# Kernel optimization log

Measured on AMD Instinct MI355X. Metric: run time of the kernel, lower is better.

## Reference

```python
import jax, jax.numpy as jnp
import numpy as np

D_MODEL = 1024
D_Q = 1024
D_K = 1024
D_V = 1024
B, S = 4, 2048


def setup_inputs() -> dict:
    key = jax.random.key(0)
    kx, kq, kk, kv = jax.random.split(key, 4)
    # torch Linear(in, out) weight is [out, in]; y = x @ W.T. Use kaiming-ish scale.
    sc = 1.0 / np.sqrt(D_MODEL)
    x = jax.random.normal(kx, (B, S, D_MODEL), dtype=jnp.float32)
    Wq = jax.random.normal(kq, (D_Q, D_MODEL), dtype=jnp.float32) * sc
    Wk = jax.random.normal(kk, (D_K, D_MODEL), dtype=jnp.float32) * sc
    Wv = jax.random.normal(kv, (D_V, D_MODEL), dtype=jnp.float32) * sc
    return {"x": x, "Wq": Wq, "Wk": Wk, "Wv": Wv}


def reference(x, Wq, Wk, Wv):
    d_k = Wk.shape[0]
    q = jnp.einsum('bsd,qd->bsq', x, Wq)  # [B,S,d_q]
    k = jnp.einsum('bsd,kd->bsk', x, Wk)  # [B,S,d_k]
    v = jnp.einsum('bsd,vd->bsv', x, Wv)  # [B,S,d_v]
    scores = jnp.einsum('bqd,bkd->bqk', q, k) / jnp.sqrt(jnp.float32(d_k))
    seq = scores.shape[-1]
    causal = jnp.tril(jnp.ones((seq, seq), dtype=bool))  # True = keep
    scores = jnp.where(causal[None, :, :], scores, -jnp.inf)
    probs = jax.nn.softmax(scores, axis=-1)
    return jnp.einsum('bqk,bkv->bqv', probs, v)
```

## Files before the change

kernel.cpp:

```cpp
#include <hip/hip_runtime.h>
#include <hip/hip_bf16.h>
#include <stdint.h>

typedef __attribute__((ext_vector_type(8))) short short8;
typedef __attribute__((ext_vector_type(4))) float floatx4;

typedef const __attribute__((address_space(1))) void* gvp;
typedef __attribute__((address_space(3))) void* lvp;

__device__ __forceinline__ unsigned short f2bf(float f) {
    unsigned u = __float_as_uint(f);
    u += 0x7fffu + ((u >> 16) & 1u);
    return (unsigned short)(u >> 16);
}

#define BAR()   do { asm volatile("" ::: "memory"); __builtin_amdgcn_s_barrier(); asm volatile("" ::: "memory"); } while (0)
#define WAITL() do { asm volatile("s_waitcnt lgkmcnt(0)" ::: "memory"); __builtin_amdgcn_sched_barrier(0); } while (0)
#define WAITV4() asm volatile("s_waitcnt vmcnt(4)" ::: "memory")
#define WAITV0() asm volatile("s_waitcnt vmcnt(0)" ::: "memory")

__global__ __launch_bounds__(256)
void cvt_all(const float* __restrict__ x, const float* __restrict__ wq,
             const float* __restrict__ wk, const float* __restrict__ wv,
             unsigned short* __restrict__ Xb, unsigned short* __restrict__ WqT,
             unsigned short* __restrict__ WkT, unsigned short* __restrict__ Wvb) {
    const int b = blockIdx.x, t = threadIdx.x;
    if (b < 2304) {
        const float* in; unsigned short* out; long base;
        if (b < 2048) { in = x;  out = Xb;  base = (long)b * 1024; }
        else          { in = wv; out = Wvb; base = (long)(b - 2048) * 1024; }
        #pragma unroll
        for (int k = 0; k < 4; ++k) {
            long idx = base + k * 256 + t;
            float4 v = reinterpret_cast<const float4*>(in)[idx];
            uint2 o;
            o.x = (unsigned)f2bf(v.x) | ((unsigned)f2bf(v.y) << 16);
            o.y = (unsigned)f2bf(v.z) | ((unsigned)f2bf(v.w) << 16);
            reinterpret_cast<uint2*>(out)[idx] = o;
        }
    } else {
        const int bb = b - 2304;
        const float* in = (bb < 256) ? wq : wk;
        unsigned short* out = (bb < 256) ? WqT : WkT;
        const int tile = bb & 255;
        const int e0 = (tile >> 4) * 64, d0 = (tile & 15) * 64;
        __shared__ unsigned short ldsT[64][68];
        const int r = t >> 4, cq = t & 15;
        #pragma unroll
        for (int p = 0; p < 4; ++p) {
            const int e = p * 16 + r;
            float4 v = *reinterpret_cast<const float4*>(in + (long)(e0 + e) * 1024 + d0 + cq * 4);
            ldsT[cq*4+0][e] = f2bf(v.x);
            ldsT[cq*4+1][e] = f2bf(v.y);
            ldsT[cq*4+2][e] = f2bf(v.z);
            ldsT[cq*4+3][e] = f2bf(v.w);
        }
        __syncthreads();
        #pragma unroll
        for (int p = 0; p < 4; ++p) {
            const int d = p * 16 + r;
            ushort4 o = *reinterpret_cast<const ushort4*>(&ldsT[d][cq * 4]);
            *reinterpret_cast<ushort4*>(out + (long)(d0 + d) * 1024 + e0 + cq * 4) = o;
        }
    }
}

__device__ __forceinline__ void stage_tile(unsigned short* Abuf, unsigned short* Bbuf,
                                           const unsigned short* A, int lda,
                                           const unsigned short* B, int ldb, int k0,
                                           int wid, int srow, int piece) {
    #pragma unroll
    for (int i = 0; i < 4; ++i) {
        const int c = wid * 4 + i;
        const int row = c * 8 + srow;
        const int cs = (piece * 16) ^ ((row & 7) << 4);
        __builtin_amdgcn_global_load_lds(
            (gvp)(reinterpret_cast<const char*>(A + (long)row * lda + k0) + cs),
            (lvp)(reinterpret_cast<char*>(Abuf) + c * 1024), 16, 0, 0);
        __builtin_amdgcn_global_load_lds(
            (gvp)(reinterpret_cast<const char*>(B + (long)row * ldb + k0) + cs),
            (lvp)(reinterpret_cast<char*>(Bbuf) + c * 1024), 16, 0, 0);
    }
}

__device__ __forceinline__ void compute_tile(floatx4 acc[4][4], const unsigned short* As,
                                             const unsigned short* Bs, int wm, int wn,
                                             int frow, int lane) {
    #pragma unroll
    for (int ks = 0; ks < 2; ++ks) {
        short8 af[4], bf[4];
        const int colb = ks * 64 + (lane >> 4) * 16;
        #pragma unroll
        for (int i = 0; i < 4; ++i) {
            const int ar = wm + i * 16 + frow;
            af[i] = *reinterpret_cast<const short8*>(
                reinterpret_cast<const char*>(As) + ar * 128 + (colb ^ ((ar & 7) << 4)));
            const int br = wn + i * 16 + frow;
            bf[i] = *reinterpret_cast<const short8*>(
                reinterpret_cast<const char*>(Bs) + br * 128 + (colb ^ ((br & 7) << 4)));
        }
        #pragma unroll
        for (int i = 0; i < 4; ++i)
            #pragma unroll
            for (int j = 0; j < 4; ++j)
                acc[i][j] = __builtin_amdgcn_mfma_f32_16x16x32_bf16(af[i], bf[j], acc[i][j], 0, 0, 0);
    }
}

__global__ __launch_bounds__(256, 2)
void g_chunk(const unsigned short* __restrict__ WkT, const unsigned short* __restrict__ WqT,
             float* __restrict__ Gw) {
    const int bx = blockIdx.x, by = blockIdx.y, bz = blockIdx.z;
    const unsigned short* A = WkT + (long)by * 128 * 1024;
    const unsigned short* B = WqT + (long)bx * 128 * 1024;

    __shared__ unsigned short As[2][128 * 64];
    __shared__ unsigned short Bs[2][128 * 64];

    const int tid = threadIdx.x, lane = tid & 63, wid = tid >> 6;
    const int srow = lane >> 3, piece = lane & 7;
    const int wm = (wid >> 1) * 64, wn = (wid & 1) * 64, frow = lane & 15;

    floatx4 acc[4][4] = {};
    const int kbase = bz * 256;

    stage_tile(As[0], Bs[0], A, 1024, B, 1024, kbase, wid, srow, piece);
    WAITV0(); BAR();
    int cur = 0;
    #pragma unroll 1
    for (int t = 0; t < 4; ++t) {
        if (t < 3)
            stage_tile(As[cur ^ 1], Bs[cur ^ 1], A, 1024, B, 1024, kbase + (t + 1) * 64,
                       wid, srow, piece);
        compute_tile(acc, As[cur], Bs[cur], wm, wn, frow, lane);
        WAITV0(); BAR();
        cur ^= 1;
    }

    float* Cb = Gw + (long)bz * (1 << 20) + (long)(by * 128) * 1024 + bx * 128;
    const int cr0 = wm + (lane >> 4) * 4;
    const int cc0 = wn + (lane & 15);
    #pragma unroll
    for (int i = 0; i < 4; ++i)
        #pragma unroll
        for (int j = 0; j < 4; ++j)
            #pragma unroll
            for (int r = 0; r < 4; ++r)
                Cb[(long)(cr0 + i * 16 + r) * 1024 + cc0 + j * 16] = acc[i][j][r];
}

__global__ __launch_bounds__(256)
void reduce_g(const float* __restrict__ Gw, unsigned short* __restrict__ Gp) {
    const long i4 = (long)blockIdx.x * 256 + threadIdx.x;
    const long M4 = (1l << 20) / 4;
    float4 a = reinterpret_cast<const float4*>(Gw)[i4];
    float4 b = reinterpret_cast<const float4*>(Gw)[i4 + M4];
    float4 c = reinterpret_cast<const float4*>(Gw)[i4 + 2 * M4];
    float4 d = reinterpret_cast<const float4*>(Gw)[i4 + 3 * M4];
    float sx = (a.x + b.x + c.x + d.x) * 0.03125f;
    float sy = (a.y + b.y + c.y + d.y) * 0.03125f;
    float sz = (a.z + b.z + c.z + d.z) * 0.03125f;
    float sw = (a.w + b.w + c.w + d.w) * 0.03125f;
    uint2 o;
    o.x = (unsigned)f2bf(sx) | ((unsigned)f2bf(sy) << 16);
    o.y = (unsigned)f2bf(sz) | ((unsigned)f2bf(sw) << 16);
    reinterpret_cast<uint2*>(Gp)[i4] = o;
}

__global__ __launch_bounds__(256, 2)
void pv_pair(const unsigned short* __restrict__ P, const unsigned short* __restrict__ Vt,
             float* __restrict__ out) {
    int flat = (blockIdx.z * 8 + blockIdx.y) * 8 + blockIdx.x;
    { int xcd = flat & 7, lid = flat >> 3; flat = xcd * 32 + lid; }
    const int bx = flat % 8;
    const int pj = (flat / 8) % 8;
    const int bz = flat / 64;

    const unsigned short* Pb = P + (long)bz * 2048 * 4096;
    const unsigned short* Bv = Vt + (long)bz * 1024 * 2048 + (long)(bx * 128) * 2048;
    float* Cb = out + (long)bz * 2048 * 1024;

    __shared__ unsigned short As[2][128 * 64];
    __shared__ unsigned short Bs[2][128 * 64];

    const int tid = threadIdx.x, lane = tid & 63, wid = tid >> 6;
    const int srow = lane >> 3, piece = lane & 7;
    const int wm = (wid >> 1) * 64, wn = (wid & 1) * 64, frow = lane & 15;

    #pragma unroll 1
    for (int j = 0; j < 2; ++j) {
        const int by = j ? 15 - pj : pj;
        const unsigned short* A = Pb + (long)by * 128 * 4096;
        const int nt = (by + 1) * 2;

        floatx4 acc[4][4] = {};
        stage_tile(As[0], Bs[0], A, 4096, Bv, 2048, 0, wid, srow, piece);
        WAITV0(); BAR();
        int cur = 0;
        #pragma unroll 1
        for (int t = 0; t < nt; ++t) {
            if (t + 1 < nt)
                stage_tile(As[cur ^ 1], Bs[cur ^ 1], A, 4096, Bv, 2048, (t + 1) * 64,
                           wid, srow, piece);
            compute_tile(acc, As[cur], Bs[cur], wm, wn, frow, lane);
            WAITV0(); BAR();
            cur ^= 1;
        }

        float* Cj = Cb + (long)(by * 128) * 1024 + bx * 128;
        const int cr0 = wm + (lane >> 4) * 4;
        const int cc0 = wn + (lane & 15);
        #pragma unroll
        for (int i = 0; i < 4; ++i)
            #pragma unroll
            for (int jj = 0; jj < 4; ++jj)
                #pragma unroll
                for (int r = 0; r < 4; ++r)
                    Cj[(long)(cr0 + i * 16 + r) * 1024 + cc0 + jj * 16] = acc[i][jj][r];
    }
}

__device__ __forceinline__ void stage_half(char* slot, const unsigned short* src,
                                           int ld, int k0, int tid) {
    #pragma unroll
    for (int r = 0; r < 2; ++r) {
        const int c = r * 512 + tid;
        const int row = c >> 3;
        const int cs = ((c & 7) * 16) ^ ((row & 7) << 4);
        const char* g = reinterpret_cast<const char*>(src + (long)row * ld + k0) + cs;
        __builtin_amdgcn_global_load_lds((gvp)g,
            (lvp)(slot + r * 8192 + (tid >> 6) * 1024), 16, 0, 0);
    }
}

__device__ __forceinline__ void load_a4(short8 a_[4][2], const char* slot, int mh,
                                        int fr, int csw0, int csw1) {
    #pragma unroll
    for (int i = 0; i < 4; ++i) {
        const int rb = (mh * 64 + i * 16 + fr) * 128;
        a_[i][0] = *reinterpret_cast<const short8*>(slot + rb + csw0);
        a_[i][1] = *reinterpret_cast<const short8*>(slot + rb + csw1);
    }
}

__device__ __forceinline__ void load_b2(short8 b_[2][2], const char* slot, int rbase,
                                        int nh, int fr, int csw0, int csw1) {
    #pragma unroll
    for (int j = 0; j < 2; ++j) {
        const int rb = (rbase + nh * 32 + j * 16 + fr) * 128;
        b_[j][0] = *reinterpret_cast<const short8*>(slot + rb + csw0);
        b_[j][1] = *reinterpret_cast<const short8*>(slot + rb + csw1);
    }
}

__device__ __forceinline__ void mfma16(floatx4 acc[8][4], short8 a_[4][2],
                                       short8 b_[2][2], int mh, int nh) {
    __builtin_amdgcn_s_setprio(1);
    #pragma unroll
    for (int i = 0; i < 4; ++i)
        #pragma unroll
        for (int j = 0; j < 2; ++j) {
            acc[mh*4+i][nh*2+j] = __builtin_amdgcn_mfma_f32_16x16x32_bf16(
                a_[i][0], b_[j][0], acc[mh*4+i][nh*2+j], 0, 0, 0);
            acc[mh*4+i][nh*2+j] = __builtin_amdgcn_mfma_f32_16x16x32_bf16(
                a_[i][1], b_[j][1], acc[mh*4+i][nh*2+j], 0, 0, 0);
        }
    __builtin_amdgcn_s_setprio(0);
}

template<typename CT, int MODE>
__global__ __launch_bounds__(512, 2)
void gemm8p(const unsigned short* __restrict__ A, const unsigned short* B,
            const unsigned short* B1, CT* __restrict__ C, unsigned short* __restrict__ Vt,
            int K, int lda, int ldb, int ldc,
            long sA, long sB, long sC, int nwg)
{
    const int gx = gridDim.x, gy = gridDim.y;
    int flat = (blockIdx.z * gy + blockIdx.y) * gx + blockIdx.x;
    {
        int xcd = flat & 7, lid = flat >> 3;
        int q = nwg >> 3, r = nwg & 7;
        flat = (xcd < r ? xcd * (q + 1) : r * (q + 1) + (xcd - r) * q) + lid;
    }
    int bx, by, bz = 0;
    bool isV = false;
    if (MODE == 1) {
        bx = flat % gx;
        int t2 = flat / gx;
        by = t2 % gy;
        bz = t2 / gy;
        if (bx > by) return;
    } else {
        if (flat >= 128) { isV = true; flat -= 128; B = B1; }
        by = flat >> 2;
        bx = flat & 3;
    }

    A += (long)bz * sA + (long)by * 256 * lda;
    B += (long)bz * sB + (long)bx * 256 * ldb;
    C += (long)bz * sC;

    __shared__ __align__(16) char lds[8 * 16384];
    #define SLOT(db, op, half) (lds + ((((db) << 1 | (op)) << 1 | (half)) * 16384))

    const int tid  = threadIdx.x;
    const int lane = tid & 63;
    const int wid  = tid >> 6;
    const int wm = wid >> 2;
    const int wn = wid & 3;
    const int bh = wn >> 1;
    const int brbase = (wn & 1) * 64;
    const int fr = lane & 15;
    const int csw0 = ((lane >> 4) * 16) ^ ((fr & 7) << 4);
    const int csw1 = (64 + (lane >> 4) * 16) ^ ((fr & 7) << 4);

    const unsigned short* Ah[2] = { A, A + 128ll * lda };
    const unsigned short* Bh[2] = { B, B + 128ll * ldb };

    const int NT = K >> 6;
    const int NI = NT >> 1;

    floatx4 acc[8][4] = {};
    short8 a_[4][2];
    short8 b_[2][2][2];

    stage_half(SLOT(0,1,0), Bh[0], ldb, 0, tid);
    stage_half(SLOT(0,1,1), Bh[1], ldb, 0, tid);
    stage_half(SLOT(0,0,0), Ah[0], lda, 0, tid);
    stage_half(SLOT(0,0,1), Ah[1], lda, 0, tid);
    stage_half(SLOT(1,1,0), Bh[0], ldb, 64, tid);
    stage_half(SLOT(1,1,1), Bh[1], ldb, 64, tid);
    WAITV4();
    BAR();

    for (int I = 0; I < NI; ++I) {
        const int kA1 = min(2*I + 1, NT - 1) * 64;
        const int kT2 = min(2*I + 2, NT - 1) * 64;
        const int kB3 = min(2*I + 3, NT - 1) * 64;

        load_a4(a_, SLOT(0,0,wm), 0, fr, csw0, csw1);
        load_b2(b_[0], SLOT(0,1,bh), brbase, 0, fr, csw0, csw1);
        stage_half(SLOT(1,0,0), Ah[0], lda, kA1, tid);
        BAR(); WAITL();
        mfma16(acc, a_, b_[0], 0, 0);
        BAR();

        load_b2(b_[1], SLOT(0,1,bh), brbase, 1, fr, csw0, csw1);
        stage_half(SLOT(1,0,1), Ah[1], lda, kA1, tid);
        BAR(); WAITL();
        mfma16(acc, a_, b_[1], 0, 1);
        BAR();

        load_a4(a_, SLOT(0,0,wm), 1, fr, csw0, csw1);
        stage_half(SLOT(0,1,0), Bh[0], ldb, kT2, tid);
        BAR(); WAITL();
        mfma16(acc, a_, b_[1], 1, 1);
        BAR();

        stage_half(SLOT(0,1,1), Bh[1], ldb, kT2, tid);
        BAR(); WAITL();
        mfma16(acc, a_, b_[0], 1, 0);
        WAITV4();
        BAR();

        load_a4(a_, SLOT(1,0,wm), 0, fr, csw0, csw1);
        load_b2(b_[0], SLOT(1,1,bh), brbase, 0, fr, csw0, csw1);
        stage_half(SLOT(0,0,0), Ah[0], lda, kT2, tid);
        BAR(); WAITL();
        mfma16(acc, a_, b_[0], 0, 0);
        BAR();

        load_b2(b_[1], SLOT(1,1,bh), brbase, 1, fr, csw0, csw1);
        stage_half(SLOT(0,0,1), Ah[1], lda, kT2, tid);
        BAR(); WAITL();
        mfma16(acc, a_, b_[1], 0, 1);
        BAR();

        load_a4(a_, SLOT(1,0,wm), 1, fr, csw0, csw1);
        stage_half(SLOT(1,1,0), Bh[0], ldb, kB3, tid);
        BAR(); WAITL();
        mfma16(acc, a_, b_[1], 1, 1);
        BAR();

        stage_half(SLOT(1,1,1), Bh[1], ldb, kB3, tid);
        BAR(); WAITL();
        mfma16(acc, a_, b_[0], 1, 0);
        WAITV4();
        BAR();
    }

    if (MODE == 3 && isV) {
        WAITV0();
        BAR();
        char* T = lds;
        #pragma unroll
        for (int i = 0; i < 8; ++i)
            #pragma unroll
            for (int j = 0; j < 4; ++j) {
                const int n = wn * 64 + j * 16 + fr;
                const int m = wm * 128 + ((lane >> 4) << 2) + i * 16;
                uint2 pk;
                pk.x = (unsigned)f2bf(acc[i][j][0]) | ((unsigned)f2bf(acc[i][j][1]) << 16);
                pk.y = (unsigned)f2bf(acc[i][j][2]) | ((unsigned)f2bf(acc[i][j][3]) << 16);
                *reinterpret_cast<uint2*>(T + n * 512 + ((m * 2) ^ ((n & 7) << 4))) = pk;
            }
        __syncthreads();
        const int b  = by >> 3;
        const int s0 = (by & 7) * 256;
        #pragma unroll
        for (int c = 0; c < 16; ++c) {
            const int idx = c * 512 + tid;
            const int n = idx >> 5, k = idx & 31;
            uint4 v = *reinterpret_cast<const uint4*>(T + n * 512 + ((k * 16) ^ ((n & 7) << 4)));
            *reinterpret_cast<uint4*>(Vt + (long)b * (1024 * 2048)
                + (long)(bx * 256 + n) * 2048 + s0 + k * 8) = v;
        }
        return;
    }

    const int cr0 = by * 256 + wm * 128 + (lane >> 4) * 4;
    const int cc0 = bx * 256 + wn * 64 + (lane & 15);
    #pragma unroll
    for (int i = 0; i < 8; ++i)
        #pragma unroll
        for (int j = 0; j < 4; ++j)
            #pragma unroll
            for (int r = 0; r < 4; ++r) {
                long idx = (long)(cr0 + i * 16 + r) * ldc + (cc0 + j * 16);
                float v = acc[i][j][r];
                if constexpr (sizeof(CT) == 4) C[idx] = v;
                else                           C[idx] = (CT)f2bf(v);
            }
    #undef SLOT
}

__global__ __launch_bounds__(256)
void softmax_causal(float* __restrict__ Sc) {
    const int q = blockIdx.x;
    const int b = blockIdx.y;
    float* row = Sc + ((long)b * 2048 + q) * 2048;
    const int t = threadIdx.x;
    const int lane = t & 63, wid = t >> 6;
    const int kend = (q | 127) + 1;

    float vals[8];
    float mx = -INFINITY;
    #pragma unroll
    for (int i = 0; i < 2; ++i) {
        const int c0 = i * 1024 + t * 4;
        if (c0 <= q) {
            float4 v = *reinterpret_cast<const float4*>(row + c0);
            float tmp[4] = {v.x, v.y, v.z, v.w};
            #pragma unroll
            for (int j = 0; j < 4; ++j) {
                float val = (c0 + j <= q) ? tmp[j] : -INFINITY;
                vals[i * 4 + j] = val;
                mx = fmaxf(mx, val);
            }
        } else {
            vals[i*4+0] = vals[i*4+1] = vals[i*4+2] = vals[i*4+3] = -INFINITY;
        }
    }
    #pragma unroll
    for (int o = 32; o > 0; o >>= 1) mx = fmaxf(mx, __shfl_xor(mx, o));
    __shared__ float rmax[4], rsum[4];
    if (lane == 0) rmax[wid] = mx;
    __syncthreads();
    mx = fmaxf(fmaxf(rmax[0], rmax[1]), fmaxf(rmax[2], rmax[3]));

    float s = 0.f;
    #pragma unroll
    for (int k = 0; k < 8; ++k) {
        float e = __expf(vals[k] - mx);
        vals[k] = e;
        s += e;
    }
    #pragma unroll
    for (int o = 32; o > 0; o >>= 1) s += __shfl_xor(s, o);
    if (lane == 0) rsum[wid] = s;
    __syncthreads();
    s = rsum[0] + rsum[1] + rsum[2] + rsum[3];
    const float inv = 1.f / s;

    unsigned short* orow = reinterpret_cast<unsigned short*>(row);
    #pragma unroll
    for (int i = 0; i < 2; ++i) {
        const int c0 = i * 1024 + t * 4;
        if (c0 < kend) {
            uint2 o;
            o.x = (unsigned)f2bf(vals[i*4+0] * inv) | ((unsigned)f2bf(vals[i*4+1] * inv) << 16);
            o.y = (unsigned)f2bf(vals[i*4+2] * inv) | ((unsigned)f2bf(vals[i*4+3] * inv) << 16);
            *reinterpret_cast<uint2*>(orow + c0) = o;
        }
    }
}

extern "C" void kernel_launch(void* const* d_in, const int* in_sizes, int n_in,
                              void* d_out, int out_size, void* d_ws, size_t ws_size,
                              hipStream_t stream) {
    const float* x  = (const float*)d_in[0];
    const float* Wq = (const float*)d_in[1];
    const float* Wk = (const float*)d_in[2];
    const float* Wv = (const float*)d_in[3];
    float* out = (float*)d_out;

    char* w = (char*)d_ws;
    unsigned short* Xb  = (unsigned short*)(w);
    unsigned short* WqT = (unsigned short*)(w + (16ll << 20));
    unsigned short* WkT = (unsigned short*)(w + (18ll << 20));
    unsigned short* Wvb = (unsigned short*)(w + (20ll << 20));
    unsigned short* Yb  = (unsigned short*)(w + (22ll << 20));
    unsigned short* Gp  = (unsigned short*)(w + (38ll << 20));
    float*          Gw  = (float*)(w + (40ll << 20));
    unsigned short* Vt  = (unsigned short*)(w + (70ll << 20));
    float* Sc = (float*)(w + (86ll << 20));

    dim3 blk(256);
    cvt_all<<<2816, blk, 0, stream>>>(x, Wq, Wk, Wv, Xb, WqT, WkT, Wvb);

    g_chunk<<<dim3(8, 8, 4), blk, 0, stream>>>(WkT, WqT, Gw);
    reduce_g<<<1024, blk, 0, stream>>>(Gw, Gp);

    gemm8p<unsigned short, 3><<<dim3(256, 1, 1), dim3(512), 0, stream>>>(
        Xb, Gp, Wvb, Yb, Vt, 1024, 1024, 1024, 1024,
        0, 0, 0, 256);

    gemm8p<float, 1><<<dim3(8, 8, 4), dim3(512), 0, stream>>>(
        Yb, Xb, nullptr, Sc, nullptr, 1024, 1024, 1024, 2048,
        2048ll * 1024, 2048ll * 1024, 2048ll * 2048, 256);

    softmax_causal<<<dim3(2048, 4), blk, 0, stream>>>(Sc);

    pv_pair<<<dim3(8, 8, 4), blk, 0, stream>>>((const unsigned short*)Sc, Vt, out);
}
```

Measured before the change: 145.3 us.

## Deepen PV pipeline to four LDS stages and pair softmax rows per block

```diff
diff --git a/kernel.cpp b/kernel.cpp
--- a/kernel.cpp
+++ b/kernel.cpp
@@ -14,10 +14,12 @@
     return (unsigned short)(u >> 16);
 }
 
-#define BAR()   do { asm volatile("" ::: "memory"); __builtin_amdgcn_s_barrier(); asm volatile("" ::: "memory"); } while (0)
-#define WAITL() do { asm volatile("s_waitcnt lgkmcnt(0)" ::: "memory"); __builtin_amdgcn_sched_barrier(0); } while (0)
+#define BAR()    do { asm volatile("" ::: "memory"); __builtin_amdgcn_s_barrier(); asm volatile("" ::: "memory"); } while (0)
+#define WAITL()  do { asm volatile("s_waitcnt lgkmcnt(0)" ::: "memory"); __builtin_amdgcn_sched_barrier(0); } while (0)
 #define WAITV4() asm volatile("s_waitcnt vmcnt(4)" ::: "memory")
 #define WAITV0() asm volatile("s_waitcnt vmcnt(0)" ::: "memory")
+#define WAITV8() asm volatile("s_waitcnt vmcnt(8)" ::: "memory")
+#define WAITV16() asm volatile("s_waitcnt vmcnt(16)" ::: "memory")
 
 __global__ __launch_bounds__(256)
 void cvt_all(const float* __restrict__ x, const float* __restrict__ wq,
@@ -167,7 +169,7 @@
     reinterpret_cast<uint2*>(Gp)[i4] = o;
 }
 
-__global__ __launch_bounds__(256, 2)
+__global__ __launch_bounds__(256, 1)
 void pv_pair(const unsigned short* __restrict__ P, const unsigned short* __restrict__ Vt,
              float* __restrict__ out) {
     int flat = (blockIdx.z * 8 + blockIdx.y) * 8 + blockIdx.x;
@@ -180,8 +182,8 @@
     const unsigned short* Bv = Vt + (long)bz * 1024 * 2048 + (long)(bx * 128) * 2048;
     float* Cb = out + (long)bz * 2048 * 1024;
 
-    __shared__ unsigned short As[2][128 * 64];
-    __shared__ unsigned short Bs[2][128 * 64];
+    __shared__ unsigned short As[4][128 * 64];
+    __shared__ unsigned short Bs[4][128 * 64];
 
     const int tid = threadIdx.x, lane = tid & 63, wid = tid >> 6;
     const int srow = lane >> 3, piece = lane & 7;
@@ -194,17 +196,25 @@
         const int nt = (by + 1) * 2;
 
         floatx4 acc[4][4] = {};
-        stage_tile(As[0], Bs[0], A, 4096, Bv, 2048, 0, wid, srow, piece);
-        WAITV0(); BAR();
-        int cur = 0;
+        stage_tile(As[0], Bs[0], A, 4096, Bv, 2048, 0,   wid, srow, piece);
+        stage_tile(As[1], Bs[1], A, 4096, Bv, 2048, 64,  wid, srow, piece);
+        stage_tile(As[2], Bs[2], A, 4096, Bv, 2048, 128, wid, srow, piece);
+        WAITV16();
+        BAR();
+
         #pragma unroll 1
         for (int t = 0; t < nt; ++t) {
-            if (t + 1 < nt)
-                stage_tile(As[cur ^ 1], Bs[cur ^ 1], A, 4096, Bv, 2048, (t + 1) * 64,
-                           wid, srow, piece);
-            compute_tile(acc, As[cur], Bs[cur], wm, wn, frow, lane);
-            WAITV0(); BAR();
-            cur ^= 1;
+            if (t + 3 < nt) {
+                stage_tile(As[(t + 3) & 3], Bs[(t + 3) & 3], A, 4096, Bv, 2048,
+                           (t + 3) * 64, wid, srow, piece);
+                compute_tile(acc, As[t & 3], Bs[t & 3], wm, wn, frow, lane);
+                WAITV16();
+            } else {
+                compute_tile(acc, As[t & 3], Bs[t & 3], wm, wn, frow, lane);
+                if (t + 2 < nt)      { WAITV8(); }
+                else                 { WAITV0(); }
+            }
+            BAR();
         }
 
         float* Cj = Cb + (long)(by * 128) * 1024 + bx * 128;
@@ -436,61 +446,65 @@
 
 __global__ __launch_bounds__(256)
 void softmax_causal(float* __restrict__ Sc) {
-    const int q = blockIdx.x;
     const int b = blockIdx.y;
-    float* row = Sc + ((long)b * 2048 + q) * 2048;
     const int t = threadIdx.x;
     const int lane = t & 63, wid = t >> 6;
-    const int kend = (q | 127) + 1;
-
-    float vals[8];
-    float mx = -INFINITY;
-    #pragma unroll
-    for (int i = 0; i < 2; ++i) {
-        const int c0 = i * 1024 + t * 4;
-        if (c0 <= q) {
-            float4 v = *reinterpret_cast<const float4*>(row + c0);
-            float tmp[4] = {v.x, v.y, v.z, v.w};
-            #pragma unroll
-            for (int j = 0; j < 4; ++j) {
-                float val = (c0 + j <= q) ? tmp[j] : -INFINITY;
-                vals[i * 4 + j] = val;
-                mx = fmaxf(mx, val);
+    __shared__ float rmax[2][4], rsum[2][4];
+
+    #pragma unroll 1
+    for (int h = 0; h < 2; ++h) {
+        const int q = h ? 2047 - blockIdx.x : blockIdx.x;
+        float* row = Sc + ((long)b * 2048 + q) * 2048;
+        const int kend = (q | 127) + 1;
+
+        float vals[8];
+        float mx = -INFINITY;
+        #pragma unroll
+        for (int i = 0; i < 2; ++i) {
+            const int c0 = i * 1024 + t * 4;
+            if (c0 <= q) {
+                float4 v = *reinterpret_cast<const float4*>(row + c0);
+                float tmp[4] = {v.x, v.y, v.z, v.w};
+                #pragma unroll
+                for (int j = 0; j < 4; ++j) {
+                    float val = (c0 + j <= q) ? tmp[j] : -INFINITY;
+                    vals[i * 4 + j] = val;
+                    mx = fmaxf(mx, val);
+                }
+            } else {
+                vals[i*4+0] = vals[i*4+1] = vals[i*4+2] = vals[i*4+3] = -INFINITY;
             }
-        } else {
-            vals[i*4+0] = vals[i*4+1] = vals[i*4+2] = vals[i*4+3] = -INFINITY;
-        }
-    }
-    #pragma unroll
-    for (int o = 32; o > 0; o >>= 1) mx = fmaxf(mx, __shfl_xor(mx, o));
-    __shared__ float rmax[4], rsum[4];
-    if (lane == 0) rmax[wid] = mx;
-    __syncthreads();
-    mx = fmaxf(fmaxf(rmax[0], rmax[1]), fmaxf(rmax[2], rmax[3]));
-
-    float s = 0.f;
-    #pragma unroll
-    for (int k = 0; k < 8; ++k) {
-        float e = __expf(vals[k] - mx);
-        vals[k] = e;
-        s += e;
-    }
-    #pragma unroll
-    for (int o = 32; o > 0; o >>= 1) s += __shfl_xor(s, o);
-    if (lane == 0) rsum[wid] = s;
-    __syncthreads();
-    s = rsum[0] + rsum[1] + rsum[2] + rsum[3];
-    const float inv = 1.f / s;
-
-    unsigned short* orow = reinterpret_cast<unsigned short*>(row);
-    #pragma unroll
-    for (int i = 0; i < 2; ++i) {
-        const int c0 = i * 1024 + t * 4;
-        if (c0 < kend) {
-            uint2 o;
-            o.x = (unsigned)f2bf(vals[i*4+0] * inv) | ((unsigned)f2bf(vals[i*4+1] * inv) << 16);
-            o.y = (unsigned)f2bf(vals[i*4+2] * inv) | ((unsigned)f2bf(vals[i*4+3] * inv) << 16);
-            *reinterpret_cast<uint2*>(orow + c0) = o;
+        }
+        #pragma unroll
+        for (int o = 32; o > 0; o >>= 1) mx = fmaxf(mx, __shfl_xor(mx, o));
+        if (lane == 0) rmax[h][wid] = mx;
+        __syncthreads();
+        mx = fmaxf(fmaxf(rmax[h][0], rmax[h][1]), fmaxf(rmax[h][2], rmax[h][3]));
+
+        float s = 0.f;
+        #pragma unroll
+        for (int k = 0; k < 8; ++k) {
+            float e = __expf(vals[k] - mx);
+            vals[k] = e;
+            s += e;
+        }
+        #pragma unroll
+        for (int o = 32; o > 0; o >>= 1) s += __shfl_xor(s, o);
+        if (lane == 0) rsum[h][wid] = s;
+        __syncthreads();
+        s = rsum[h][0] + rsum[h][1] + rsum[h][2] + rsum[h][3];
+        const float inv = 1.f / s;
+
+        unsigned short* orow = reinterpret_cast<unsigned short*>(row);
+        #pragma unroll
+        for (int i = 0; i < 2; ++i) {
+            const int c0 = i * 1024 + t * 4;
+            if (c0 < kend) {
+                uint2 o;
+                o.x = (unsigned)f2bf(vals[i*4+0] * inv) | ((unsigned)f2bf(vals[i*4+1] * inv) << 16);
+                o.y = (unsigned)f2bf(vals[i*4+2] * inv) | ((unsigned)f2bf(vals[i*4+3] * inv) << 16);
+                *reinterpret_cast<uint2*>(orow + c0) = o;
+            }
         }
     }
 }
@@ -529,7 +543,7 @@
         Yb, Xb, nullptr, Sc, nullptr, 1024, 1024, 1024, 2048,
         2048ll * 1024, 2048ll * 1024, 2048ll * 2048, 256);
 
-    softmax_causal<<<dim3(2048, 4), blk, 0, stream>>>(Sc);
+    softmax_causal<<<dim3(1024, 4), blk, 0, stream>>>(Sc);
 
     pv_pair<<<dim3(8, 8, 4), blk, 0, stream>>>((const unsigned short*)Sc, Vt, out);
 }
```

Result: slower. 150.9 us (+3.8%).

## Remap tiles to XCDs for L2 locality and pair softmax rows for balance

Applied to the files above, without the earlier changes.

```diff
diff --git a/kernel.cpp b/kernel.cpp
--- a/kernel.cpp
+++ b/kernel.cpp
@@ -14,8 +14,8 @@
     return (unsigned short)(u >> 16);
 }
 
-#define BAR()   do { asm volatile("" ::: "memory"); __builtin_amdgcn_s_barrier(); asm volatile("" ::: "memory"); } while (0)
-#define WAITL() do { asm volatile("s_waitcnt lgkmcnt(0)" ::: "memory"); __builtin_amdgcn_sched_barrier(0); } while (0)
+#define BAR()    do { asm volatile("" ::: "memory"); __builtin_amdgcn_s_barrier(); asm volatile("" ::: "memory"); } while (0)
+#define WAITL()  do { asm volatile("s_waitcnt lgkmcnt(0)" ::: "memory"); __builtin_amdgcn_sched_barrier(0); } while (0)
 #define WAITV4() asm volatile("s_waitcnt vmcnt(4)" ::: "memory")
 #define WAITV0() asm volatile("s_waitcnt vmcnt(0)" ::: "memory")
 
@@ -170,11 +170,11 @@
 __global__ __launch_bounds__(256, 2)
 void pv_pair(const unsigned short* __restrict__ P, const unsigned short* __restrict__ Vt,
              float* __restrict__ out) {
-    int flat = (blockIdx.z * 8 + blockIdx.y) * 8 + blockIdx.x;
-    { int xcd = flat & 7, lid = flat >> 3; flat = xcd * 32 + lid; }
-    const int bx = flat % 8;
-    const int pj = (flat / 8) % 8;
-    const int bz = flat / 64;
+    const int flat = (blockIdx.z * 8 + blockIdx.y) * 8 + blockIdx.x;
+    const int xcd = flat & 7, lid = flat >> 3;
+    const int bz = xcd >> 1;
+    const int bx = (xcd & 1) * 4 + (lid & 3);
+    const int pj = lid >> 2;
 
     const unsigned short* Pb = P + (long)bz * 2048 * 4096;
     const unsigned short* Bv = Vt + (long)bz * 1024 * 2048 + (long)(bx * 128) * 2048;
@@ -277,23 +277,24 @@
 {
     const int gx = gridDim.x, gy = gridDim.y;
     int flat = (blockIdx.z * gy + blockIdx.y) * gx + blockIdx.x;
-    {
+    int bx, by, bz = 0;
+    bool isV = false;
+    if (MODE == 1) {
         int xcd = flat & 7, lid = flat >> 3;
         int q = nwg >> 3, r = nwg & 7;
         flat = (xcd < r ? xcd * (q + 1) : r * (q + 1) + (xcd - r) * q) + lid;
-    }
-    int bx, by, bz = 0;
-    bool isV = false;
-    if (MODE == 1) {
         bx = flat % gx;
         int t2 = flat / gx;
         by = t2 % gy;
         bz = t2 / gy;
         if (bx > by) return;
     } else {
-        if (flat >= 128) { isV = true; flat -= 128; B = B1; }
-        by = flat >> 2;
-        bx = flat & 3;
+        const int xcd = flat & 7, lid = flat >> 3;
+        by = xcd + ((lid >> 3) << 3);
+        const int sub = lid & 7;
+        isV = (sub >> 2) != 0;
+        bx = sub & 3;
+        if (isV) B = B1;
     }
 
     A += (long)bz * sA + (long)by * 256 * lda;
@@ -436,61 +437,65 @@
 
 __global__ __launch_bounds__(256)
 void softmax_causal(float* __restrict__ Sc) {
-    const int q = blockIdx.x;
     const int b = blockIdx.y;
-    float* row = Sc + ((long)b * 2048 + q) * 2048;
     const int t = threadIdx.x;
     const int lane = t & 63, wid = t >> 6;
-    const int kend = (q | 127) + 1;
-
-    float vals[8];
-    float mx = -INFINITY;
-    #pragma unroll
-    for (int i = 0; i < 2; ++i) {
-        const int c0 = i * 1024 + t * 4;
-        if (c0 <= q) {
-            float4 v = *reinterpret_cast<const float4*>(row + c0);
-            float tmp[4] = {v.x, v.y, v.z, v.w};
-            #pragma unroll
-            for (int j = 0; j < 4; ++j) {
-                float val = (c0 + j <= q) ? tmp[j] : -INFINITY;
-                vals[i * 4 + j] = val;
-                mx = fmaxf(mx, val);
+    __shared__ float rmax[2][4], rsum[2][4];
+
+    #pragma unroll 1
+    for (int h = 0; h < 2; ++h) {
+        const int q = h ? 2047 - blockIdx.x : blockIdx.x;
+        float* row = Sc + ((long)b * 2048 + q) * 2048;
+        const int kend = (q | 127) + 1;
+
+        float vals[8];
+        float mx = -INFINITY;
+        #pragma unroll
+        for (int i = 0; i < 2; ++i) {
+            const int c0 = i * 1024 + t * 4;
+            if (c0 <= q) {
+                float4 v = *reinterpret_cast<const float4*>(row + c0);
+                float tmp[4] = {v.x, v.y, v.z, v.w};
+                #pragma unroll
+                for (int j = 0; j < 4; ++j) {
+                    float val = (c0 + j <= q) ? tmp[j] : -INFINITY;
+                    vals[i * 4 + j] = val;
+                    mx = fmaxf(mx, val);
+                }
+            } else {
+                vals[i*4+0] = vals[i*4+1] = vals[i*4+2] = vals[i*4+3] = -INFINITY;
             }
-        } else {
-            vals[i*4+0] = vals[i*4+1] = vals[i*4+2] = vals[i*4+3] = -INFINITY;
-        }
-    }
-    #pragma unroll
-    for (int o = 32; o > 0; o >>= 1) mx = fmaxf(mx, __shfl_xor(mx, o));
-    __shared__ float rmax[4], rsum[4];
-    if (lane == 0) rmax[wid] = mx;
-    __syncthreads();
-    mx = fmaxf(fmaxf(rmax[0], rmax[1]), fmaxf(rmax[2], rmax[3]));
-
-    float s = 0.f;
-    #pragma unroll
-    for (int k = 0; k < 8; ++k) {
-        float e = __expf(vals[k] - mx);
-        vals[k] = e;
-        s += e;
-    }
-    #pragma unroll
-    for (int o = 32; o > 0; o >>= 1) s += __shfl_xor(s, o);
-    if (lane == 0) rsum[wid] = s;
-    __syncthreads();
-    s = rsum[0] + rsum[1] + rsum[2] + rsum[3];
-    const float inv = 1.f / s;
-
-    unsigned short* orow = reinterpret_cast<unsigned short*>(row);
-    #pragma unroll
-    for (int i = 0; i < 2; ++i) {
-        const int c0 = i * 1024 + t * 4;
-        if (c0 < kend) {
-            uint2 o;
-            o.x = (unsigned)f2bf(vals[i*4+0] * inv) | ((unsigned)f2bf(vals[i*4+1] * inv) << 16);
-            o.y = (unsigned)f2bf(vals[i*4+2] * inv) | ((unsigned)f2bf(vals[i*4+3] * inv) << 16);
-            *reinterpret_cast<uint2*>(orow + c0) = o;
+        }
+        #pragma unroll
+        for (int o = 32; o > 0; o >>= 1) mx = fmaxf(mx, __shfl_xor(mx, o));
+        if (lane == 0) rmax[h][wid] = mx;
+        __syncthreads();
+        mx = fmaxf(fmaxf(rmax[h][0], rmax[h][1]), fmaxf(rmax[h][2], rmax[h][3]));
+
+        float s = 0.f;
+        #pragma unroll
+        for (int k = 0; k < 8; ++k) {
+            float e = __expf(vals[k] - mx);
+            vals[k] = e;
+            s += e;
+        }
+        #pragma unroll
+        for (int o = 32; o > 0; o >>= 1) s += __shfl_xor(s, o);
+        if (lane == 0) rsum[h][wid] = s;
+        __syncthreads();
+        s = rsum[h][0] + rsum[h][1] + rsum[h][2] + rsum[h][3];
+        const float inv = 1.f / s;
+
+        unsigned short* orow = reinterpret_cast<unsigned short*>(row);
+        #pragma unroll
+        for (int i = 0; i < 2; ++i) {
+            const int c0 = i * 1024 + t * 4;
+            if (c0 < kend) {
+                uint2 o;
+                o.x = (unsigned)f2bf(vals[i*4+0] * inv) | ((unsigned)f2bf(vals[i*4+1] * inv) << 16);
+                o.y = (unsigned)f2bf(vals[i*4+2] * inv) | ((unsigned)f2bf(vals[i*4+3] * inv) << 16);
+                *reinterpret_cast<uint2*>(orow + c0) = o;
+            }
         }
     }
 }
@@ -529,7 +534,7 @@
         Yb, Xb, nullptr, Sc, nullptr, 1024, 1024, 1024, 2048,
         2048ll * 1024, 2048ll * 1024, 2048ll * 2048, 256);
 
-    softmax_causal<<<dim3(2048, 4), blk, 0, stream>>>(Sc);
+    softmax_causal<<<dim3(1024, 4), blk, 0, stream>>>(Sc);
 
     pv_pair<<<dim3(8, 8, 4), blk, 0, stream>>>((const unsigned short*)Sc, Vt, out);
 }
```

After: 143.7 us. No clear change (-1.1%).
